# Optimization experiments

Hardware: AMD Instinct MI355X
Metric: run time of the kernel (lower is better)

## Reference

```python
import jax, jax.numpy as jnp
import numpy as np
from jax import lax

B, L, D, K = 4, 4096, 2048, 4
EPS = 1e-5


def setup_inputs() -> dict:
    key = jax.random.key(0)
    k1, k2, k3 = jax.random.split(key, 3)
    x = jax.random.normal(k1, (B, L, D), dtype=jnp.float32)
    # RMSNorm learned scale (torch nn.RMSNorm weight), perturbed around 1
    norm_weight = 1.0 + 0.02 * jax.random.normal(k2, (D,), dtype=jnp.float32)
    # depthwise conv weight in jax 'WIO' layout: (K, 1, D). torch layout is (D, 1, K).
    conv_weight = 0.1 * jax.random.normal(k3, (K, 1, D), dtype=jnp.float32)
    return {"x": x, "norm_weight": norm_weight, "conv_weight": conv_weight}


def reference(x, norm_weight, conv_weight):
    # RMSNorm over last dim: x / sqrt(mean(x^2) + eps) * weight
    ms = jnp.mean(jnp.square(x), axis=-1, keepdims=True)
    x_norm = x * lax.rsqrt(ms + EPS) * norm_weight  # (B, L, D)

    # Depthwise causal conv1d: left-pad K-1 zeros along L (equivalent to
    # torch's symmetric padding=(K-1) followed by [..., :L] slice).
    y = lax.conv_general_dilated(
        x_norm,                     # (B, L, D)
        conv_weight,                # (K, 1, D)
        window_strides=(1,),
        padding=[(K - 1, 0)],
        dimension_numbers=("NWC", "WIO", "NWC"),
        feature_group_count=D,
    )                               # (B, L, D)

    # SiLU activation
    return y * jax.nn.sigmoid(y)
```

## Files before the change

kernel.cpp:

```cpp
#include <hip/hip_runtime.h>

constexpr int B = 4;
constexpr int L = 4096;
constexpr int D = 2048;
constexpr float EPS = 1e-5f;

constexpr int CL = 16;
constexpr int NR = CL + 3;
constexpr int NW = 8;
constexpr int NCHUNK = L / CL;
constexpr int NWG = NCHUNK * B;

typedef float floatx4 __attribute__((ext_vector_type(4)));

__global__ __launch_bounds__(512, 4) void fused_kernel(const float* __restrict__ x,
                                                       const float* __restrict__ nw,
                                                       const float* __restrict__ cw,
                                                       float* __restrict__ out) {
    const int t = threadIdx.x;
    const int wave = t >> 6;
    const int lane = t & 63;

    const int bid = blockIdx.x;
    const int swz = (bid & 7) * (NWG / 8) + (bid >> 3);
    const int b = swz / NCHUNK;
    const int chunk = swz % NCHUNK;
    const int l0 = chunk * CL;
    const int d = t * 4;

    const float* xb = x + (size_t)b * L * D + d;
    float* ob = out + (size_t)b * L * D + d;

    __shared__ __align__(16) float s_red[NR][NW];

    const floatx4 nwv = *reinterpret_cast<const floatx4*>(nw + d);
    floatx4 wn[4];
    #pragma unroll
    for (int k = 0; k < 4; ++k)
        wn[k] = *reinterpret_cast<const floatx4*>(cw + k * D + d) * nwv;

    floatx4 hx[NR];
    #pragma unroll
    for (int j = 0; j < NR; ++j) {
        const int l = l0 - 3 + j;
        if (l >= 0)
            hx[j] = *reinterpret_cast<const floatx4*>(xb + (size_t)l * D);
        else
            hx[j] = (floatx4)0.0f;
    }

    #pragma unroll
    for (int j = 0; j < NR; ++j) {
        float s = hx[j].x * hx[j].x + hx[j].y * hx[j].y
                + hx[j].z * hx[j].z + hx[j].w * hx[j].w;
        #pragma unroll
        for (int off = 32; off > 0; off >>= 1)
            s += __shfl_down(s, off, 64);
        if (lane == 0) s_red[j][wave] = s;
    }

    __syncthreads();

    #pragma unroll
    for (int j = 0; j < NR; ++j) {
        floatx4 p0 = *reinterpret_cast<const floatx4*>(&s_red[j][0]);
        floatx4 p1 = *reinterpret_cast<const floatx4*>(&s_red[j][4]);
        float tot = ((p0.x + p0.y) + (p0.z + p0.w))
                  + ((p1.x + p1.y) + (p1.z + p1.w));
        const float irms = rsqrtf(tot * (1.0f / D) + EPS);
        hx[j] *= irms;
    }

    #pragma unroll
    for (int li = 0; li < CL; ++li) {
        floatx4 y = wn[0] * hx[li]     + wn[1] * hx[li + 1]
                  + wn[2] * hx[li + 2] + wn[3] * hx[li + 3];
        floatx4 sg;
        sg.x = 1.0f / (1.0f + __expf(-y.x));
        sg.y = 1.0f / (1.0f + __expf(-y.y));
        sg.z = 1.0f / (1.0f + __expf(-y.z));
        sg.w = 1.0f / (1.0f + __expf(-y.w));
        y *= sg;
        __builtin_nontemporal_store(y,
            reinterpret_cast<floatx4*>(ob + (size_t)(l0 + li) * D));
    }
}

extern "C" void kernel_launch(void* const* d_in, const int* in_sizes, int n_in,
                              void* d_out, int out_size, void* d_ws, size_t ws_size,
                              hipStream_t stream) {
    const float* x  = (const float*)d_in[0];
    const float* nw = (const float*)d_in[1];
    const float* cw = (const float*)d_in[2];
    float* out = (float*)d_out;

    fused_kernel<<<NWG, 512, 0, stream>>>(x, nw, cw, out);
}
```

Baseline: 52.88 us.

## Split RMS reduction into separate kernel and halve conv chunk length

Result: slower. 64.15 us (+21.3%).

```diff
diff --git a/kernel.cpp b/kernel.cpp
--- a/kernel.cpp
+++ b/kernel.cpp
@@ -5,24 +5,46 @@
 constexpr int D = 2048;
 constexpr float EPS = 1e-5f;
 
-constexpr int CL = 16;
+constexpr int CL = 8;
 constexpr int NR = CL + 3;
-constexpr int NW = 8;
 constexpr int NCHUNK = L / CL;
-constexpr int NWG = NCHUNK * B;
+constexpr int NWG2 = NCHUNK * B;
 
 typedef float floatx4 __attribute__((ext_vector_type(4)));
 
-__global__ __launch_bounds__(512, 4) void fused_kernel(const float* __restrict__ x,
-                                                       const float* __restrict__ nw,
-                                                       const float* __restrict__ cw,
-                                                       float* __restrict__ out) {
+__global__ __launch_bounds__(256) void rms_kernel(const float* __restrict__ x,
+                                                  float* __restrict__ inv_rms) {
+    const int wave = threadIdx.x >> 6;
+    const int lane = threadIdx.x & 63;
+    const int row = blockIdx.x * 4 + wave;
+
+    const floatx4* xr = reinterpret_cast<const floatx4*>(x + (size_t)row * D);
+
+    floatx4 v[8];
+    #pragma unroll
+    for (int i = 0; i < 8; ++i) v[i] = xr[lane + i * 64];
+
+    float s = 0.0f;
+    #pragma unroll
+    for (int i = 0; i < 8; ++i)
+        s += v[i].x * v[i].x + v[i].y * v[i].y + v[i].z * v[i].z + v[i].w * v[i].w;
+
+    #pragma unroll
+    for (int off = 32; off > 0; off >>= 1)
+        s += __shfl_down(s, off, 64);
+
+    if (lane == 0)
+        inv_rms[row] = rsqrtf(s * (1.0f / D) + EPS);
+}
+
+__global__ __launch_bounds__(512) void conv_kernel(const float* __restrict__ x,
+                                                   const float* __restrict__ nw,
+                                                   const float* __restrict__ cw,
+                                                   const float* __restrict__ inv_rms,
+                                                   float* __restrict__ out) {
     const int t = threadIdx.x;
-    const int wave = t >> 6;
-    const int lane = t & 63;
-
     const int bid = blockIdx.x;
-    const int swz = (bid & 7) * (NWG / 8) + (bid >> 3);
+    const int swz = (bid & 7) * (NWG2 / 8) + (bid >> 3);
     const int b = swz / NCHUNK;
     const int chunk = swz % NCHUNK;
     const int l0 = chunk * CL;
@@ -30,8 +52,7 @@
 
     const float* xb = x + (size_t)b * L * D + d;
     float* ob = out + (size_t)b * L * D + d;
-
-    __shared__ __align__(16) float s_red[NR][NW];
+    const float* ir = inv_rms + (size_t)b * L;
 
     const floatx4 nwv = *reinterpret_cast<const floatx4*>(nw + d);
     floatx4 wn[4];
@@ -49,27 +70,14 @@
             hx[j] = (floatx4)0.0f;
     }
 
+    float irv[NR];
     #pragma unroll
     for (int j = 0; j < NR; ++j) {
-        float s = hx[j].x * hx[j].x + hx[j].y * hx[j].y
-                + hx[j].z * hx[j].z + hx[j].w * hx[j].w;
-        #pragma unroll
-        for (int off = 32; off > 0; off >>= 1)
-            s += __shfl_down(s, off, 64);
-        if (lane == 0) s_red[j][wave] = s;
+        const int l = l0 - 3 + j;
+        irv[j] = (l >= 0) ? ir[l] : 0.0f;
     }
-
-    __syncthreads();
-
     #pragma unroll
-    for (int j = 0; j < NR; ++j) {
-        floatx4 p0 = *reinterpret_cast<const floatx4*>(&s_red[j][0]);
-        floatx4 p1 = *reinterpret_cast<const floatx4*>(&s_red[j][4]);
-        float tot = ((p0.x + p0.y) + (p0.z + p0.w))
-                  + ((p1.x + p1.y) + (p1.z + p1.w));
-        const float irms = rsqrtf(tot * (1.0f / D) + EPS);
-        hx[j] *= irms;
-    }
+    for (int j = 0; j < NR; ++j) hx[j] *= irv[j];
 
     #pragma unroll
     for (int li = 0; li < CL; ++li) {
@@ -93,6 +101,8 @@
     const float* nw = (const float*)d_in[1];
     const float* cw = (const float*)d_in[2];
     float* out = (float*)d_out;
+    float* inv_rms = (float*)d_ws;
 
-    fused_kernel<<<NWG, 512, 0, stream>>>(x, nw, cw, out);
+    rms_kernel<<<B * L / 4, 256, 0, stream>>>(x, inv_rms);
+    conv_kernel<<<NWG2, 512, 0, stream>>>(x, nw, cw, inv_rms, out);
 }
```

## Pipeline chunk processing in row groups with register prefetch and lighter barriers

Applied to the files above, without the earlier changes.

New measurement: 51.24 us. 1.03x faster.

```diff
diff --git a/kernel.cpp b/kernel.cpp
--- a/kernel.cpp
+++ b/kernel.cpp
@@ -5,13 +5,24 @@
 constexpr int D = 2048;
 constexpr float EPS = 1e-5f;
 
-constexpr int CL = 16;
-constexpr int NR = CL + 3;
+constexpr int CL = 32;
+constexpr int R  = 8;
+constexpr int NG = CL / R;
 constexpr int NW = 8;
 constexpr int NCHUNK = L / CL;
 constexpr int NWG = NCHUNK * B;
 
 typedef float floatx4 __attribute__((ext_vector_type(4)));
+
+__device__ __forceinline__ void light_barrier() {
+    asm volatile("s_waitcnt lgkmcnt(0)" ::: "memory");
+    __builtin_amdgcn_s_barrier();
+    asm volatile("" ::: "memory");
+}
+
+__device__ __forceinline__ float dot4(floatx4 v) {
+    return v.x * v.x + v.y * v.y + v.z * v.z + v.w * v.w;
+}
 
 __global__ __launch_bounds__(512, 4) void fused_kernel(const float* __restrict__ x,
                                                        const float* __restrict__ nw,
@@ -31,7 +42,7 @@
     const float* xb = x + (size_t)b * L * D + d;
     float* ob = out + (size_t)b * L * D + d;
 
-    __shared__ __align__(16) float s_red[NR][NW];
+    __shared__ __align__(16) float s_red[2][R][NW];
 
     const floatx4 nwv = *reinterpret_cast<const floatx4*>(nw + d);
     floatx4 wn[4];
@@ -39,50 +50,96 @@
     for (int k = 0; k < 4; ++k)
         wn[k] = *reinterpret_cast<const floatx4*>(cw + k * D + d) * nwv;
 
-    floatx4 hx[NR];
+    floatx4 hx[3];
     #pragma unroll
-    for (int j = 0; j < NR; ++j) {
+    for (int j = 0; j < 3; ++j) {
         const int l = l0 - 3 + j;
+        hx[j] = (floatx4)0.0f;
         if (l >= 0)
             hx[j] = *reinterpret_cast<const floatx4*>(xb + (size_t)l * D);
-        else
-            hx[j] = (floatx4)0.0f;
+    }
+    floatx4 cur[R], nxt[R];
+    #pragma unroll
+    for (int r = 0; r < R; ++r)
+        cur[r] = *reinterpret_cast<const floatx4*>(xb + (size_t)(l0 + r) * D);
+
+    float win_x[3], win_y[3], win_z[3], win_w[3];
+    {
+        #pragma unroll
+        for (int j = 0; j < 3; ++j) {
+            float s = dot4(hx[j]);
+            #pragma unroll
+            for (int off = 32; off > 0; off >>= 1)
+                s += __shfl_down(s, off, 64);
+            if (lane == 0) s_red[0][j][wave] = s;
+        }
+        light_barrier();
+        #pragma unroll
+        for (int j = 0; j < 3; ++j) {
+            floatx4 p0 = *reinterpret_cast<const floatx4*>(&s_red[0][j][0]);
+            floatx4 p1 = *reinterpret_cast<const floatx4*>(&s_red[0][j][4]);
+            float tot = ((p0.x + p0.y) + (p0.z + p0.w))
+                      + ((p1.x + p1.y) + (p1.z + p1.w));
+            const float irms = rsqrtf(tot * (1.0f / D) + EPS);
+            floatx4 c = hx[j] * irms;
+            win_x[j] = c.x; win_y[j] = c.y; win_z[j] = c.z; win_w[j] = c.w;
+        }
     }
 
-    #pragma unroll
-    for (int j = 0; j < NR; ++j) {
-        float s = hx[j].x * hx[j].x + hx[j].y * hx[j].y
-                + hx[j].z * hx[j].z + hx[j].w * hx[j].w;
+    #pragma unroll 1
+    for (int g = 0; g < NG; ++g) {
+        const int par = (g + 1) & 1;
+
+        if (g + 1 < NG) {
+            #pragma unroll
+            for (int r = 0; r < R; ++r)
+                nxt[r] = *reinterpret_cast<const floatx4*>(
+                             xb + (size_t)(l0 + (g + 1) * R + r) * D);
+        }
+
         #pragma unroll
-        for (int off = 32; off > 0; off >>= 1)
-            s += __shfl_down(s, off, 64);
-        if (lane == 0) s_red[j][wave] = s;
-    }
+        for (int r = 0; r < R; ++r) {
+            float s = dot4(cur[r]);
+            #pragma unroll
+            for (int off = 32; off > 0; off >>= 1)
+                s += __shfl_down(s, off, 64);
+            if (lane == 0) s_red[par][r][wave] = s;
+        }
 
-    __syncthreads();
+        light_barrier();
 
-    #pragma unroll
-    for (int j = 0; j < NR; ++j) {
-        floatx4 p0 = *reinterpret_cast<const floatx4*>(&s_red[j][0]);
-        floatx4 p1 = *reinterpret_cast<const floatx4*>(&s_red[j][4]);
-        float tot = ((p0.x + p0.y) + (p0.z + p0.w))
-                  + ((p1.x + p1.y) + (p1.z + p1.w));
-        const float irms = rsqrtf(tot * (1.0f / D) + EPS);
-        hx[j] *= irms;
-    }
+        #pragma unroll
+        for (int r = 0; r < R; ++r) {
+            floatx4 p0 = *reinterpret_cast<const floatx4*>(&s_red[par][r][0]);
+            floatx4 p1 = *reinterpret_cast<const floatx4*>(&s_red[par][r][4]);
+            float tot = ((p0.x + p0.y) + (p0.z + p0.w))
+                      + ((p1.x + p1.y) + (p1.z + p1.w));
+            const float irms = rsqrtf(tot * (1.0f / D) + EPS);
+            floatx4 c = cur[r] * irms;
 
-    #pragma unroll
-    for (int li = 0; li < CL; ++li) {
-        floatx4 y = wn[0] * hx[li]     + wn[1] * hx[li + 1]
-                  + wn[2] * hx[li + 2] + wn[3] * hx[li + 3];
-        floatx4 sg;
-        sg.x = 1.0f / (1.0f + __expf(-y.x));
-        sg.y = 1.0f / (1.0f + __expf(-y.y));
-        sg.z = 1.0f / (1.0f + __expf(-y.z));
-        sg.w = 1.0f / (1.0f + __expf(-y.w));
-        y *= sg;
-        __builtin_nontemporal_store(y,
-            reinterpret_cast<floatx4*>(ob + (size_t)(l0 + li) * D));
+            floatx4 y;
+            y.x = wn[0].x * win_x[0] + wn[1].x * win_x[1] + wn[2].x * win_x[2] + wn[3].x * c.x;
+            y.y = wn[0].y * win_y[0] + wn[1].y * win_y[1] + wn[2].y * win_y[2] + wn[3].y * c.y;
+            y.z = wn[0].z * win_z[0] + wn[1].z * win_z[1] + wn[2].z * win_z[2] + wn[3].z * c.z;
+            y.w = wn[0].w * win_w[0] + wn[1].w * win_w[1] + wn[2].w * win_w[2] + wn[3].w * c.w;
+
+            floatx4 sg;
+            sg.x = 1.0f / (1.0f + __expf(-y.x));
+            sg.y = 1.0f / (1.0f + __expf(-y.y));
+            sg.z = 1.0f / (1.0f + __expf(-y.z));
+            sg.w = 1.0f / (1.0f + __expf(-y.w));
+            y *= sg;
+            __builtin_nontemporal_store(y,
+                reinterpret_cast<floatx4*>(ob + (size_t)(l0 + g * R + r) * D));
+
+            win_x[0] = win_x[1]; win_x[1] = win_x[2]; win_x[2] = c.x;
+            win_y[0] = win_y[1]; win_y[1] = win_y[2]; win_y[2] = c.y;
+            win_z[0] = win_z[1]; win_z[1] = win_z[2]; win_z[2] = c.z;
+            win_w[0] = win_w[1]; win_w[1] = win_w[2]; win_w[2] = c.w;
+        }
+
+        #pragma unroll
+        for (int r = 0; r < R; ++r) cur[r] = nxt[r];
     }
 }
 
```
